# Kernel tuning notes

Hardware: AMD Instinct MI355X
Metric: run time of the kernel (lower is better)

The kernel has to match this reference:

```python
import jax, jax.numpy as jnp
import numpy as np
from jax import lax

N_QUBITS = 4
N_QLAYERS = 2
C64 = jnp.complex64
PAIRS = [(i, j) for i in range(N_QUBITS) for j in range(i + 1, N_QUBITS)]  # 6 entangling pairs
CNOT = jnp.array([[1, 0, 0, 0], [0, 1, 0, 0], [0, 0, 0, 1], [0, 0, 1, 0]], dtype=C64)


def _rx(t):
    c = jnp.cos(t / 2).astype(C64)
    s = (-1j * jnp.sin(t / 2)).astype(C64)
    return jnp.stack([jnp.stack([c, s]), jnp.stack([s, c])])


def _ry(t):
    c = jnp.cos(t / 2).astype(C64)
    s = jnp.sin(t / 2).astype(C64)
    return jnp.stack([jnp.stack([c, -s]), jnp.stack([s, c])])


def _rz(t):
    e = jnp.exp(-1j * t.astype(C64) / 2)
    z = jnp.zeros_like(e)
    return jnp.stack([jnp.stack([e, z]), jnp.stack([z, jnp.conj(e)])])


def _apply_1q(state, M, w):
    # state: (B,2,2,2,2); M: (2,2) shared or (B,2,2) per-sample
    s = jnp.moveaxis(state, 1 + w, -1)
    if M.ndim == 2:
        s = jnp.einsum('b...j,ij->b...i', s, M)
    else:
        s = jnp.einsum('b...j,bij->b...i', s, M)
    return jnp.moveaxis(s, -1, 1 + w)


def _apply_2q(state, M4, c, t):
    # M4: (4,4) acting on (wire c, wire t)
    s = jnp.moveaxis(state, (1 + c, 1 + t), (-2, -1))
    sh = s.shape
    s = s.reshape(sh[:-2] + (4,))
    s = jnp.einsum('b...j,ij->b...i', s, M4)
    s = s.reshape(sh)
    return jnp.moveaxis(s, (-2, -1), (1 + c, 1 + t))


def _quantum_batched(angles, q_params):
    # angles: (B, 4) classical outputs; encoding is RY(angles*pi)
    B = angles.shape[0]
    state = jnp.zeros((B, 16), C64).at[:, 0].set(1.0).reshape(B, 2, 2, 2, 2)
    theta = angles * jnp.float32(np.pi)
    c = jnp.cos(theta / 2).astype(C64)  # (B,4)
    s = jnp.sin(theta / 2).astype(C64)
    for w in range(N_QUBITS):
        M = jnp.stack([jnp.stack([c[:, w], -s[:, w]], -1),
                       jnp.stack([s[:, w], c[:, w]], -1)], -2)  # (B,2,2)
        state = _apply_1q(state, M, w)
    per_layer = 3 * N_QUBITS + len(PAIRS)  # 18
    for l in range(N_QLAYERS):
        start = l * per_layer
        rot = q_params[start:start + 3 * N_QUBITS].reshape(N_QUBITS, 3)
        ent = q_params[start + 3 * N_QUBITS:start + per_layer]
        for q in range(N_QUBITS):
            M = _rz(rot[q, 2]) @ _ry(rot[q, 1]) @ _rx(rot[q, 0])
            state = _apply_1q(state, M, q)
        for k, (i, j) in enumerate(PAIRS):
            M4 = jnp.kron(jnp.eye(2, dtype=C64), _rz(ent[k])) @ CNOT  # CNOT then RZ on target
            state = _apply_2q(state, M4, i, j)
    probs = jnp.abs(state) ** 2  # (B,2,2,2,2)
    signs = jnp.array([1.0, -1.0], jnp.float32)
    zs = []
    for w in range(N_QUBITS):
        pw = jnp.moveaxis(probs, 1 + w, -1).reshape(B, -1, 2)
        zs.append((pw.sum(1) * signs).sum(-1))
    return jnp.stack(zs, -1)  # (B,4) PauliZ expvals


def _conv(x, w, b):
    y = lax.conv_general_dilated(x, w, (1, 1), ((1, 1), (1, 1)),
                                 dimension_numbers=('NCHW', 'OIHW', 'NCHW'))
    return y + b[None, :, None, None]


def _pool(x):
    return lax.reduce_window(x, -jnp.inf, lax.max, (1, 1, 2, 2), (1, 1, 2, 2), 'VALID')


def setup_inputs() -> dict:
    key = jax.random.key(0)
    ks = jax.random.split(key, 10)
    B = 4096
    return {
        'x': jax.random.normal(ks[0], (B, 1, 28, 28), jnp.float32),
        'conv1_w': jax.random.normal(ks[1], (16, 1, 3, 3), jnp.float32) * 0.1,
        'conv1_b': jax.random.normal(ks[2], (16,), jnp.float32) * 0.1,
        'conv2_w': jax.random.normal(ks[3], (32, 16, 3, 3), jnp.float32) * 0.05,
        'conv2_b': jax.random.normal(ks[4], (32,), jnp.float32) * 0.1,
        'dense_w': jax.random.normal(ks[5], (4, 1568), jnp.float32) * 0.02,
        'dense_b': jax.random.normal(ks[6], (4,), jnp.float32) * 0.1,
        'q_params': jax.random.normal(ks[7], (36,), jnp.float32) * 0.1,
        'post_w': jax.random.normal(ks[8], (10, 4), jnp.float32) * 0.5,
        'post_b': jax.random.normal(ks[9], (10,), jnp.float32) * 0.1,
    }


def reference(x, conv1_w, conv1_b, conv2_w, conv2_b, dense_w, dense_b, q_params, post_w, post_b):
    h = jax.nn.relu(_conv(x, conv1_w, conv1_b))
    h = _pool(h)
    h = jax.nn.relu(_conv(h, conv2_w, conv2_b))
    h = _pool(h)  # (B,32,7,7)
    h = h.reshape(h.shape[0], 32 * 7 * 7)
    # dropout is identity in eval mode
    angles = h @ dense_w.T + dense_b  # (B,4)
    z = _quantum_batched(angles, q_params)  # (B,4)
    return z @ post_w.T + post_b  # (B,10)
```

## Files before the change

### kernel.cpp

```cpp
#include <hip/hip_runtime.h>

#define PI_F 3.14159265358979323846f

typedef _Float16 half2v __attribute__((ext_vector_type(2)));
typedef _Float16 half4v __attribute__((ext_vector_type(4)));
typedef _Float16 half8v __attribute__((ext_vector_type(8)));
typedef float f32x4 __attribute__((ext_vector_type(4)));

struct C2 { float x, y; };
__device__ __forceinline__ C2 cmul(C2 a, C2 b) {
    return C2{a.x * b.x - a.y * b.y, a.x * b.y + a.y * b.x};
}

__device__ __forceinline__ void gate1(float& re, float& im, int l, int w,
                                      C2 m00, C2 m01, C2 m10, C2 m11) {
    int mask = 1 << (3 - w);
    float pre = __shfl_xor(re, mask, 64);
    float pim = __shfl_xor(im, mask, 64);
    bool b = (l & mask) != 0;
    C2 d = b ? m11 : m00;
    C2 o = b ? m10 : m01;
    float nre = d.x * re - d.y * im + o.x * pre - o.y * pim;
    float nim = d.x * im + d.y * re + o.x * pim + o.y * pre;
    re = nre; im = nim;
}

#define P1_PIX 272
#define P1_SEL (P1_PIX * 8)

#define WS_C1B 2560
#define WS_DWT 2688
#define WS_GROT 8960
#define WS_GENT 9024

__global__ __launch_bounds__(256) void qnn_prep(
    const float* __restrict__ w1g, const float* __restrict__ w2g,
    const float* __restrict__ dwg, const float* __restrict__ qpg,
    float* __restrict__ ws)
{
    int t = threadIdx.x;
    for (int e = t; e < 640; e += 256) {
        int kstep = e >> 7, rem = e & 127;
        int ntile = rem >> 6, lane = rem & 63;
        int kq = lane >> 4, n = lane & 15;
        int oc = ntile * 16 + n;
        int pi = kstep * 2 + (kq >> 1);
        half8v h;
        #pragma unroll
        for (int jj = 0; jj < 8; ++jj) {
            int ic = (kq & 1) * 8 + jj;
            float v = (pi < 9) ? w2g[oc * 144 + ic * 9 + pi] : 0.f;
            h[jj] = (_Float16)v;
        }
        *(float4*)(ws + e * 4) = __builtin_bit_cast(float4, h);
    }
    if (t < 64) {
        int ky = t >> 4, n = t & 15;
        half4v h;
        #pragma unroll
        for (int j = 0; j < 4; ++j) {
            float v = (ky < 3 && j < 3) ? w1g[n * 9 + ky * 3 + j] : 0.f;
            h[j] = (_Float16)v;
        }
        *(float2*)(ws + WS_C1B + t * 2) = __builtin_bit_cast(float2, h);
    }
    for (int e = t; e < 1568; e += 256) {
        float4 v = {dwg[e], dwg[1568 + e], dwg[3136 + e], dwg[4704 + e]};
        *(float4*)(ws + WS_DWT + e * 4) = v;
    }
    if (t < 8) {
        int layer = t >> 2, q = t & 3;
        int st = layer * 18;
        float a0 = qpg[st + 3 * q], a1 = qpg[st + 3 * q + 1], a2 = qpg[st + 3 * q + 2];
        float cx = cosf(0.5f * a0), sx = sinf(0.5f * a0);
        float cy = cosf(0.5f * a1), sy = sinf(0.5f * a1);
        float cz = cosf(0.5f * a2), sz = sinf(0.5f * a2);
        C2 T00{cy * cx,  sy * sx}, T01{-sy * cx, -cy * sx};
        C2 T10{sy * cx, -cy * sx}, T11{ cy * cx, -sy * sx};
        C2 E0{cz, -sz}, E1{cz, sz};
        C2 m00 = cmul(E0, T00), m01 = cmul(E0, T01);
        C2 m10 = cmul(E1, T10), m11 = cmul(E1, T11);
        float* gm = ws + WS_GROT + t * 8;
        gm[0] = m00.x; gm[1] = m00.y; gm[2] = m01.x; gm[3] = m01.y;
        gm[4] = m10.x; gm[5] = m10.y; gm[6] = m11.x; gm[7] = m11.y;
    }
    if (t >= 32 && t < 44) {
        int k = t - 32;
        float e = qpg[(k / 6) * 18 + 12 + (k % 6)];
        ws[WS_GENT + k * 2]     = cosf(0.5f * e);
        ws[WS_GENT + k * 2 + 1] = sinf(0.5f * e);
    }
}

__global__ __launch_bounds__(256, 6) void qnn_fused(
    const float* __restrict__ xg,
    const float* __restrict__ b1g, const float* __restrict__ b2g,
    const float* __restrict__ dbg,
    const float* __restrict__ wsc,
    const float* __restrict__ pwg, const float* __restrict__ pbg,
    float* __restrict__ out)
{
    const int b = blockIdx.x;
    const int t = threadIdx.x;
    const int lane = t & 63;
    const int wv = __builtin_amdgcn_readfirstlane(t >> 6);
    const int kq = lane >> 4;
    const int lm = lane & 15;

    __shared__ __align__(16) unsigned xp[932];
    __shared__ __align__(16) _Float16 p1f[2 * P1_SEL];
    __shared__ __align__(16) float angp[16];

    half8v bC2[5][2];
    {
        const float4* wsB = (const float4*)wsc;
        #pragma unroll
        for (int ks = 0; ks < 5; ++ks)
            #pragma unroll
            for (int nt = 0; nt < 2; ++nt)
                bC2[ks][nt] = __builtin_bit_cast(half8v, wsB[(ks * 2 + nt) * 64 + lane]);
    }
    half4v bC1 = __builtin_bit_cast(half4v, *(const float2*)(wsc + WS_C1B + lane * 2));
    float bias1 = b1g[lm];
    float b20 = b2g[lm], b21 = b2g[16 + lm];

    const float* xb = xg + (size_t)b * 784;
    {
        int y = t / 30, x = t - y * 30;
        for (int i = t; i < 930; i += 256) {
            bool in1 = (y >= 1 && y <= 28 && x >= 1 && x <= 28);
            float v1 = in1 ? xb[(y - 1) * 28 + (x - 1)] : 0.f;
            int y2 = y, x2 = x + 1;
            if (x2 == 30) { x2 = 0; y2 = y + 1; }
            bool in2 = (y2 >= 1 && y2 <= 28 && x2 >= 1 && x2 <= 28);
            float v2 = in2 ? xb[(y2 - 1) * 28 + (x2 - 1)] : 0.f;
            half2v p;
            p.x = (_Float16)v1;
            p.y = (_Float16)v2;
            xp[i] = __builtin_bit_cast(unsigned, p);
            x += 16; y += 8; if (x >= 30) { x -= 30; y += 1; }
        }
        if (t < 2) xp[930 + t] = 0u;
    }
    {
        uint4 z4 = {0u, 0u, 0u, 0u};
        uint4* p4 = (uint4*)p1f;
        #pragma unroll
        for (int j = 0; j < 3; ++j) {
            int i = t + j * 256;
            if (i < 544) p4[i] = z4;
        }
    }
    __syncthreads();

    {
        int kyc = (kq < 3) ? kq : 0;
        int pos = lm & 3;
        int pyo = pos >> 1, pxo = pos & 1;
        int p14 = wv * 4 + (lm >> 2);
        int Y = p14 / 14, X = p14 - Y * 14;
        int q14 = wv * 4 + kq;
        int r = q14 / 14, c = q14 - r * 14;
        for (int tile = wv; tile < 49; tile += 4) {
            int py = 2 * Y + pyo, px = 2 * X + pxo;
            int base = (py + kyc) * 30 + px;
            uint2 u = {xp[base], xp[base + 2]};
            half4v a = __builtin_bit_cast(half4v, u);
            f32x4 acc = {bias1, bias1, bias1, bias1};
            acc = __builtin_amdgcn_mfma_f32_16x16x16f16(a, bC1, acc, 0, 0, 0);
            float v = fmaxf(fmaxf(acc.x, acc.y), fmaxf(acc.z, acc.w));
            v = fmaxf(v, 0.f);
            int pixw = (r + 1) * 17 + (c + 1);
            p1f[(lm >> 3) * P1_SEL + pixw * 8 + (lm & 7)] = (_Float16)v;
            X += 2; Y += 1; if (X >= 14) { X -= 14; Y += 1; }
            c += 2; r += 1; if (c >= 14) { c -= 14; r += 1; }
        }
    }
    __syncthreads();

    {
        float dp0 = 0.f, dp1 = 0.f, dp2 = 0.f, dp3 = 0.f;
        const float4* dt = (const float4*)(wsc + WS_DWT);
        const _Float16* pfs = p1f + (kq & 1) * P1_SEL;
        for (int tile = wv; tile < 13; tile += 4) {
            int m = tile * 16 + lm;
            int quad = m >> 2; if (quad > 48) quad = 48;
            int pos = m & 3;
            int Y = quad / 7, X = quad - Y * 7;
            int py = 2 * Y + (pos >> 1), px = 2 * X + (pos & 1);
            int pixb = py * 17 + px;
            f32x4 acc0 = {b20, b20, b20, b20};
            f32x4 acc1 = {b21, b21, b21, b21};
            #pragma unroll
            for (int ks = 0; ks < 5; ++ks) {
                int pi = ks * 2 + (kq >> 1);
                if (pi > 8) pi = 8;
                int ky = (pi >= 6) ? 2 : ((pi >= 3) ? 1 : 0);
                int kx = pi - ky * 3;
                half8v a = *(const half8v*)(&pfs[(pixb + ky * 17 + kx) * 8]);
                acc0 = __builtin_amdgcn_mfma_f32_16x16x32_f16(a, bC2[ks][0], acc0, 0, 0, 0);
                acc1 = __builtin_amdgcn_mfma_f32_16x16x32_f16(a, bC2[ks][1], acc1, 0, 0, 0);
            }
            int quadO = tile * 4 + kq;
            if (quadO < 49) {
                float v0 = fmaxf(fmaxf(fmaxf(acc0.x, acc0.y), fmaxf(acc0.z, acc0.w)), 0.f);
                float v1 = fmaxf(fmaxf(fmaxf(acc1.x, acc1.y), fmaxf(acc1.z, acc1.w)), 0.f);
                float4 q0 = dt[lm * 49 + quadO];
                float4 q1 = dt[(16 + lm) * 49 + quadO];
                dp0 = fmaf(v0, q0.x, fmaf(v1, q1.x, dp0));
                dp1 = fmaf(v0, q0.y, fmaf(v1, q1.y, dp1));
                dp2 = fmaf(v0, q0.z, fmaf(v1, q1.z, dp2));
                dp3 = fmaf(v0, q0.w, fmaf(v1, q1.w, dp3));
            }
        }
        #pragma unroll
        for (int m = 32; m >= 1; m >>= 1) {
            dp0 += __shfl_xor(dp0, m, 64);
            dp1 += __shfl_xor(dp1, m, 64);
            dp2 += __shfl_xor(dp2, m, 64);
            dp3 += __shfl_xor(dp3, m, 64);
        }
        if (lane == 0) {
            float4 dpv = {dp0, dp1, dp2, dp3};
            *(float4*)&angp[wv * 4] = dpv;
        }
    }
    __syncthreads();

    if (t < 64) {
        float4 a0v = *(const float4*)&angp[0];
        float4 a1v = *(const float4*)&angp[4];
        float4 a2v = *(const float4*)&angp[8];
        float4 a3v = *(const float4*)&angp[12];
        float aw[4] = {a0v.x + a1v.x + a2v.x + a3v.x + dbg[0],
                       a0v.y + a1v.y + a2v.y + a3v.y + dbg[1],
                       a0v.z + a1v.z + a2v.z + a3v.z + dbg[2],
                       a0v.w + a1v.w + a2v.w + a3v.w + dbg[3]};
        int l = t & 15;
        float re = (l == 0) ? 1.f : 0.f;
        float im = 0.f;
        #pragma unroll
        for (int w = 0; w < 4; ++w) {
            float th = aw[w] * (PI_F * 0.5f);
            float c = cosf(th), s = sinf(th);
            gate1(re, im, l, w, C2{c, 0.f}, C2{-s, 0.f}, C2{s, 0.f}, C2{c, 0.f});
        }
        #pragma unroll
        for (int layer = 0; layer < 2; ++layer) {
            #pragma unroll
            for (int q = 0; q < 4; ++q) {
                const float* gm = wsc + WS_GROT + (layer * 4 + q) * 8;
                gate1(re, im, l, q, C2{gm[0], gm[1]}, C2{gm[2], gm[3]},
                                     C2{gm[4], gm[5]}, C2{gm[6], gm[7]});
            }
            const int pi_[6] = {0, 0, 0, 1, 1, 2};
            const int pj_[6] = {1, 2, 3, 2, 3, 3};
            #pragma unroll
            for (int k = 0; k < 6; ++k) {
                int i = pi_[k], j = pj_[k];
                const float* em = wsc + WS_GENT + (layer * 6 + k) * 2;
                float ce = em[0], se = em[1];
                int maskj = 1 << (3 - j);
                float pre = __shfl_xor(re, maskj, 64);
                float pim = __shfl_xor(im, maskj, 64);
                bool bi = ((l >> (3 - i)) & 1) != 0;
                re = bi ? pre : re;
                im = bi ? pim : im;
                bool bj = (l & maskj) != 0;
                C2 ph{ce, bj ? se : -se};
                C2 r = cmul(C2{re, im}, ph);
                re = r.x; im = r.y;
            }
        }
        float pr = re * re + im * im;
        float z0 = ((l >> 3) & 1) ? -pr : pr;
        float z1 = ((l >> 2) & 1) ? -pr : pr;
        float z2 = ((l >> 1) & 1) ? -pr : pr;
        float z3 = (l & 1)        ? -pr : pr;
        #pragma unroll
        for (int m = 1; m <= 8; m <<= 1) {
            z0 += __shfl_xor(z0, m, 64);
            z1 += __shfl_xor(z1, m, 64);
            z2 += __shfl_xor(z2, m, 64);
            z3 += __shfl_xor(z3, m, 64);
        }
        if (t < 10) {
            float4 pw4 = *(const float4*)(pwg + t * 4);
            float o = pbg[t];
            o = fmaf(z0, pw4.x, o); o = fmaf(z1, pw4.y, o);
            o = fmaf(z2, pw4.z, o); o = fmaf(z3, pw4.w, o);
            out[(size_t)b * 10 + t] = o;
        }
    }
}

extern "C" void kernel_launch(void* const* d_in, const int* in_sizes, int n_in,
                              void* d_out, int out_size, void* d_ws, size_t ws_size,
                              hipStream_t stream) {
    const float* x  = (const float*)d_in[0];
    const float* w1 = (const float*)d_in[1];
    const float* b1 = (const float*)d_in[2];
    const float* w2 = (const float*)d_in[3];
    const float* b2 = (const float*)d_in[4];
    const float* dw = (const float*)d_in[5];
    const float* db = (const float*)d_in[6];
    const float* qp = (const float*)d_in[7];
    const float* pw = (const float*)d_in[8];
    const float* pb = (const float*)d_in[9];
    float* out = (float*)d_out;
    float* ws  = (float*)d_ws;
    int B = in_sizes[0] / 784;

    qnn_prep<<<1, 256, 0, stream>>>(w1, w2, dw, qp, ws);
    qnn_fused<<<B, 256, 0, stream>>>(x, b1, b2, db, ws, pw, pb, out);
}
```

Measured before the change: 117.9 us.

## Run fused QNN kernel as a single wavefront per sample, dropping block barriers

Shrinks the per-sample block from four waves to one 64-thread wave. That wave does all conv1 tiles, conv2 tiles and the dense dot products, then reduces with wave shuffles only. This removes the three __syncthreads barriers and the LDS array used for the cross-wave angle reduction. The cost is four times more serial work per wave, and the per-block LDS footprint now holds a single wave. That can cap resident waves per CU and weaken latency hiding.

```diff
diff --git a/kernel.cpp b/kernel.cpp
--- a/kernel.cpp
+++ b/kernel.cpp
@@ -92,7 +92,7 @@
     }
 }
 
-__global__ __launch_bounds__(256, 6) void qnn_fused(
+__global__ __launch_bounds__(64, 4) void qnn_fused(
     const float* __restrict__ xg,
     const float* __restrict__ b1g, const float* __restrict__ b2g,
     const float* __restrict__ dbg,
@@ -102,14 +102,11 @@
 {
     const int b = blockIdx.x;
     const int t = threadIdx.x;
-    const int lane = t & 63;
-    const int wv = __builtin_amdgcn_readfirstlane(t >> 6);
-    const int kq = lane >> 4;
-    const int lm = lane & 15;
+    const int kq = t >> 4;
+    const int lm = t & 15;
 
     __shared__ __align__(16) unsigned xp[932];
     __shared__ __align__(16) _Float16 p1f[2 * P1_SEL];
-    __shared__ __align__(16) float angp[16];
 
     half8v bC2[5][2];
     {
@@ -118,16 +115,16 @@
         for (int ks = 0; ks < 5; ++ks)
             #pragma unroll
             for (int nt = 0; nt < 2; ++nt)
-                bC2[ks][nt] = __builtin_bit_cast(half8v, wsB[(ks * 2 + nt) * 64 + lane]);
-    }
-    half4v bC1 = __builtin_bit_cast(half4v, *(const float2*)(wsc + WS_C1B + lane * 2));
+                bC2[ks][nt] = __builtin_bit_cast(half8v, wsB[(ks * 2 + nt) * 64 + t]);
+    }
+    half4v bC1 = __builtin_bit_cast(half4v, *(const float2*)(wsc + WS_C1B + t * 2));
     float bias1 = b1g[lm];
     float b20 = b2g[lm], b21 = b2g[16 + lm];
 
     const float* xb = xg + (size_t)b * 784;
     {
         int y = t / 30, x = t - y * 30;
-        for (int i = t; i < 930; i += 256) {
+        for (int i = t; i < 930; i += 64) {
             bool in1 = (y >= 1 && y <= 28 && x >= 1 && x <= 28);
             float v1 = in1 ? xb[(y - 1) * 28 + (x - 1)] : 0.f;
             int y2 = y, x2 = x + 1;
@@ -138,7 +135,7 @@
             p.x = (_Float16)v1;
             p.y = (_Float16)v2;
             xp[i] = __builtin_bit_cast(unsigned, p);
-            x += 16; y += 8; if (x >= 30) { x -= 30; y += 1; }
+            x += 4; y += 2; if (x >= 30) { x -= 30; y += 1; }
         }
         if (t < 2) xp[930 + t] = 0u;
     }
@@ -146,22 +143,19 @@
         uint4 z4 = {0u, 0u, 0u, 0u};
         uint4* p4 = (uint4*)p1f;
         #pragma unroll
-        for (int j = 0; j < 3; ++j) {
-            int i = t + j * 256;
+        for (int j = 0; j < 9; ++j) {
+            int i = t + j * 64;
             if (i < 544) p4[i] = z4;
         }
     }
-    __syncthreads();
 
     {
         int kyc = (kq < 3) ? kq : 0;
         int pos = lm & 3;
         int pyo = pos >> 1, pxo = pos & 1;
-        int p14 = wv * 4 + (lm >> 2);
-        int Y = p14 / 14, X = p14 - Y * 14;
-        int q14 = wv * 4 + kq;
-        int r = q14 / 14, c = q14 - r * 14;
-        for (int tile = wv; tile < 49; tile += 4) {
+        int X = lm >> 2, Y = 0;
+        int cc = kq, rr = 0;
+        for (int tile = 0; tile < 49; ++tile) {
             int py = 2 * Y + pyo, px = 2 * X + pxo;
             int base = (py + kyc) * 30 + px;
             uint2 u = {xp[base], xp[base + 2]};
@@ -170,24 +164,24 @@
             acc = __builtin_amdgcn_mfma_f32_16x16x16f16(a, bC1, acc, 0, 0, 0);
             float v = fmaxf(fmaxf(acc.x, acc.y), fmaxf(acc.z, acc.w));
             v = fmaxf(v, 0.f);
-            int pixw = (r + 1) * 17 + (c + 1);
+            int pixw = (rr + 1) * 17 + (cc + 1);
             p1f[(lm >> 3) * P1_SEL + pixw * 8 + (lm & 7)] = (_Float16)v;
-            X += 2; Y += 1; if (X >= 14) { X -= 14; Y += 1; }
-            c += 2; r += 1; if (c >= 14) { c -= 14; r += 1; }
-        }
-    }
-    __syncthreads();
-
-    {
-        float dp0 = 0.f, dp1 = 0.f, dp2 = 0.f, dp3 = 0.f;
+            X += 4; if (X >= 14) { X -= 14; Y += 1; }
+            cc += 4; if (cc >= 14) { cc -= 14; rr += 1; }
+        }
+    }
+
+    float dp0 = 0.f, dp1 = 0.f, dp2 = 0.f, dp3 = 0.f;
+    {
         const float4* dt = (const float4*)(wsc + WS_DWT);
         const _Float16* pfs = p1f + (kq & 1) * P1_SEL;
-        for (int tile = wv; tile < 13; tile += 4) {
-            int m = tile * 16 + lm;
-            int quad = m >> 2; if (quad > 48) quad = 48;
-            int pos = m & 3;
-            int Y = quad / 7, X = quad - Y * 7;
-            int py = 2 * Y + (pos >> 1), px = 2 * X + (pos & 1);
+        int pos = lm & 3;
+        int X = lm >> 2, Y = 0;
+        int quad = lm >> 2;
+        for (int tile = 0; tile < 13; ++tile) {
+            int Xc = X, Yc = Y;
+            if (quad > 48) { Xc = 6; Yc = 6; }
+            int py = 2 * Yc + (pos >> 1), px = 2 * Xc + (pos & 1);
             int pixb = py * 17 + px;
             f32x4 acc0 = {b20, b20, b20, b20};
             f32x4 acc1 = {b21, b21, b21, b21};
@@ -212,6 +206,8 @@
                 dp2 = fmaf(v0, q0.z, fmaf(v1, q1.z, dp2));
                 dp3 = fmaf(v0, q0.w, fmaf(v1, q1.w, dp3));
             }
+            X += 4; if (X >= 7) { X -= 7; Y += 1; }
+            quad += 4;
         }
         #pragma unroll
         for (int m = 32; m >= 1; m >>= 1) {
@@ -220,22 +216,10 @@
             dp2 += __shfl_xor(dp2, m, 64);
             dp3 += __shfl_xor(dp3, m, 64);
         }
-        if (lane == 0) {
-            float4 dpv = {dp0, dp1, dp2, dp3};
-            *(float4*)&angp[wv * 4] = dpv;
-        }
-    }
-    __syncthreads();
-
-    if (t < 64) {
-        float4 a0v = *(const float4*)&angp[0];
-        float4 a1v = *(const float4*)&angp[4];
-        float4 a2v = *(const float4*)&angp[8];
-        float4 a3v = *(const float4*)&angp[12];
-        float aw[4] = {a0v.x + a1v.x + a2v.x + a3v.x + dbg[0],
-                       a0v.y + a1v.y + a2v.y + a3v.y + dbg[1],
-                       a0v.z + a1v.z + a2v.z + a3v.z + dbg[2],
-                       a0v.w + a1v.w + a2v.w + a3v.w + dbg[3]};
+    }
+
+    {
+        float aw[4] = {dp0 + dbg[0], dp1 + dbg[1], dp2 + dbg[2], dp3 + dbg[3]};
         int l = t & 15;
         float re = (l == 0) ? 1.f : 0.f;
         float im = 0.f;
@@ -312,5 +296,5 @@
     int B = in_sizes[0] / 784;
 
     qnn_prep<<<1, 256, 0, stream>>>(w1, w2, dw, qp, ws);
-    qnn_fused<<<B, 256, 0, stream>>>(x, b1, b2, db, ws, pw, pb, out);
-}
+    qnn_fused<<<B, 64, 0, stream>>>(x, b1, b2, db, ws, pw, pb, out);
+}
```

Measured after the change: 129.0 us. 9.5% more time.
